# Kernel optimization log

Hardware: AMD Instinct MI355X
Metric: run time of the kernel (lower is better)

The kernel has to match this reference:

```python
import jax, jax.numpy as jnp
import numpy as np

D_DEC = 256  # decoder_size; W columns are [decoder | encoder] per the torch concat order


def setup_inputs() -> dict:
    key = jax.random.key(0)
    k1, k2, k3, k4 = jax.random.split(key, 4)
    B, S, E, D, A = 32, 4096, 256, 256, 256
    decoder_hidden = jax.random.normal(k1, (1, B, D), dtype=jnp.float32)
    encoder_outputs = jax.random.normal(k2, (S, B, E), dtype=jnp.float32)
    W = jax.random.normal(k3, (A, D + E), dtype=jnp.float32) / np.sqrt(D + E)
    b = jax.random.normal(k4, (A,), dtype=jnp.float32) * 0.02
    return {"decoder_hidden": decoder_hidden, "encoder_outputs": encoder_outputs, "W": W, "b": b}


def reference(decoder_hidden, encoder_outputs, W, b):
    # decoder_hidden: [1,B,D] -> [B,D]; encoder_outputs: [S,B,E] -> [B,S,E]
    dh = decoder_hidden[0]
    eo = jnp.transpose(encoder_outputs, (1, 0, 2))
    # Split the concat-linear: cat([dec, enc]) @ W.T == dec @ Wd.T + enc @ We.T
    Wd, We = W[:, :D_DEC], W[:, D_DEC:]
    # scores: tanh(linear) summed over attn dim -> [B,S]
    proj = dh @ Wd.T + b  # [B,A]
    attn = jnp.tanh(proj[:, None, :] + jnp.einsum('bse,ae->bsa', eo, We))
    scores = jnp.sum(attn, axis=2)  # [B,S]
    attn_softmax = jax.nn.softmax(scores, axis=1)  # [B,S]
    attended = jnp.einsum('bs,bse->be', attn_softmax, eo)  # [B,E]
    encoder_norms = jnp.linalg.norm(eo, axis=2)  # [B,S]
    attn_map = attn_softmax * encoder_norms
    return attended, attn_map
```

## Files before the change

### kernel.cpp

```cpp
#include <hip/hip_runtime.h>
#include <math.h>

#define B_  32
#define S_  4096
#define E_  256
#define A_  256
#define DE_ 512

typedef __attribute__((ext_vector_type(8))) short short8;
typedef __attribute__((ext_vector_type(4))) float f32x4;

__device__ inline unsigned short f2bf(float x) {
    unsigned int u = __float_as_uint(x);
    u += 0x7FFFu + ((u >> 16) & 1u);
    return (unsigned short)(u >> 16);
}
__device__ inline float tanh_fast(float x) {
    x = fminf(fmaxf(x, -15.f), 15.f);
    float t = __expf(2.f * x);
    return (t - 1.f) * __builtin_amdgcn_rcpf(t + 1.f);
}

__device__ __forceinline__ void conv_write(float4 v0, float4 v1,
                                           unsigned short* buf, int eu,
                                           unsigned short* rt,
                                           float& nacc)
{
    nacc += v0.x*v0.x + v0.y*v0.y + v0.z*v0.z + v0.w*v0.w
          + v1.x*v1.x + v1.y*v1.y + v1.z*v1.z + v1.w*v1.w;
    float xs[8] = {v0.x, v0.y, v0.z, v0.w, v1.x, v1.y, v1.z, v1.w};
    unsigned int hp[4], lp[4], rp[4];
    #pragma unroll
    for (int j = 0; j < 4; ++j) {
        unsigned int u0 = __float_as_uint(xs[2*j])   & 0xFFFF0000u;
        unsigned int u1 = __float_as_uint(xs[2*j+1]) & 0xFFFF0000u;
        hp[j] = (u0 >> 16) | u1;
        lp[j] = (unsigned int)f2bf(xs[2*j]   - __uint_as_float(u0))
              | ((unsigned int)f2bf(xs[2*j+1] - __uint_as_float(u1)) << 16);
        rp[j] = (unsigned int)f2bf(xs[2*j])
              | ((unsigned int)f2bf(xs[2*j+1]) << 16);
    }
    *(uint4*)&buf[(size_t)eu * 8]         = make_uint4(hp[0], hp[1], hp[2], hp[3]);
    *(uint4*)&buf[(size_t)(264 + eu) * 8] = make_uint4(lp[0], lp[1], lp[2], lp[3]);
    *(uint4*)&rt[(size_t)eu * 8]          = make_uint4(rp[0], rp[1], rp[2], rp[3]);
}

__global__ __launch_bounds__(256) void prep_kernel(
    const float* __restrict__ W, const float* __restrict__ dh,
    const float* __restrict__ bias, unsigned short* __restrict__ wepk,
    float* __restrict__ proj)
{
    __shared__ float dh_lds[E_];
    const int bk  = blockIdx.x;
    const int tid = threadIdx.x;
    if (bk < 64) {
        const int idx = bk * 256 + tid;
        const int c     = idx >> 11;
        const int r     = idx & 2047;
        const int plane = r >> 10;
        const int kg    = (r >> 8) & 3;
        const int a     = r & 255;
        const float* src = W + (size_t)a * DE_ + E_ + c * 32 + kg * 8;
        unsigned int pk[4];
        #pragma unroll
        for (int j = 0; j < 4; ++j) {
            float x0 = src[2 * j], x1 = src[2 * j + 1];
            unsigned int u0 = __float_as_uint(x0) & 0xFFFF0000u;
            unsigned int u1 = __float_as_uint(x1) & 0xFFFF0000u;
            if (plane) {
                unsigned short l0 = f2bf(x0 - __uint_as_float(u0));
                unsigned short l1 = f2bf(x1 - __uint_as_float(u1));
                pk[j] = (unsigned int)l0 | ((unsigned int)l1 << 16);
            } else {
                pk[j] = (u0 >> 16) | u1;
            }
        }
        *(uint4*)&wepk[(size_t)idx * 8] = make_uint4(pk[0], pk[1], pk[2], pk[3]);
    } else {
        const int b = bk - 64;
        const int a = tid;
        dh_lds[a] = dh[b * E_ + a];
        __syncthreads();
        float acc = bias[a];
        const float* wrow = W + (size_t)a * DE_;
        #pragma unroll
        for (int d = 0; d < E_; d += 4) {
            float4 w = *(const float4*)(wrow + d);
            acc += dh_lds[d] * w.x + dh_lds[d+1] * w.y
                 + dh_lds[d+2] * w.z + dh_lds[d+3] * w.w;
        }
        proj[b * A_ + a] = acc;
    }
}

__global__ __launch_bounds__(256, 3) void scores_kernel(
    const float* __restrict__ eo, const unsigned short* __restrict__ wepk,
    const float* __restrict__ proj,
    float* __restrict__ scores, float* __restrict__ nsq,
    float* __restrict__ Pbuf)
{
    __shared__ __align__(16) unsigned char pool[52736];
    unsigned short* eo_hl  = (unsigned short*)pool;
    unsigned short* retain = (unsigned short*)(pool + 18944);

    const int tid = threadIdx.x;
    const int b   = blockIdx.x & (B_ - 1);
    const int s0  = (blockIdx.x >> 5) * 64;
    const int w   = tid >> 6, l = tid & 63;
    const int lq  = l >> 4,  lr = l & 15;

    const int erow = tid >> 2;
    const int ekg  = tid & 3;
    const float* ebase = eo + (size_t)(s0 + erow) * (B_ * E_) + b * E_ + ekg * 8;
    const int eu = ekg * 66 + erow;

    const int wunit = lq * 256 + w * 64 + lr;

    f32x4 acc[4][4];
    #pragma unroll
    for (int i = 0; i < 4; ++i)
        #pragma unroll
        for (int j = 0; j < 4; ++j)
            acc[i][j] = (f32x4){0.f, 0.f, 0.f, 0.f};
    float nacc = 0.f;

    float pr[4];
    #pragma unroll
    for (int nt = 0; nt < 4; ++nt) pr[nt] = proj[b * A_ + w * 64 + nt * 16 + lr];

    {
        float4 v0 = *(const float4*)(ebase);
        float4 v1 = *(const float4*)(ebase + 4);
        conv_write(v0, v1, eo_hl, eu, retain, nacc);
    }
    float4 va0 = *(const float4*)(ebase + 32);
    float4 va1 = *(const float4*)(ebase + 36);
    __syncthreads();

    for (int c = 0; c < 8; ++c) {
        const int p = c & 1;
        unsigned short* rb = eo_hl + (size_t)p * 528 * 8;
        unsigned short* wb = eo_hl + (size_t)(1 - p) * 528 * 8;

        short8 bh[4], bl[4];
        {
            const unsigned short* wsrc = wepk + (size_t)(c * 2048 + wunit) * 8;
            #pragma unroll
            for (int nt = 0; nt < 4; ++nt) {
                bh[nt] = *(const short8*)(wsrc + (size_t)(nt * 16) * 8);
                bl[nt] = *(const short8*)(wsrc + (size_t)(1024 + nt * 16) * 8);
            }
        }
        short8 ah[2], al[2];
        #pragma unroll
        for (int mt = 0; mt < 2; ++mt) {
            const int au = lq * 66 + mt * 16 + lr;
            ah[mt] = *(const short8*)&rb[(size_t)au * 8];
            al[mt] = *(const short8*)&rb[(size_t)(264 + au) * 8];
        }
        if (c < 7) conv_write(va0, va1, wb, eu,
                              retain + (size_t)(c + 1) * 264 * 8, nacc);
        if (c < 6) {
            va0 = *(const float4*)(ebase + (c + 2) * 32);
            va1 = *(const float4*)(ebase + (c + 2) * 32 + 4);
        }
        #pragma unroll
        for (int mt = 0; mt < 2; ++mt) {
            #pragma unroll
            for (int nt = 0; nt < 4; ++nt) {
                acc[mt][nt] = __builtin_amdgcn_mfma_f32_16x16x32_bf16(ah[mt], bh[nt], acc[mt][nt], 0, 0, 0);
                acc[mt][nt] = __builtin_amdgcn_mfma_f32_16x16x32_bf16(ah[mt], bl[nt], acc[mt][nt], 0, 0, 0);
                acc[mt][nt] = __builtin_amdgcn_mfma_f32_16x16x32_bf16(al[mt], bh[nt], acc[mt][nt], 0, 0, 0);
            }
        }
        #pragma unroll
        for (int mt = 2; mt < 4; ++mt) {
            const int au = lq * 66 + mt * 16 + lr;
            short8 ah2 = *(const short8*)&rb[(size_t)au * 8];
            short8 al2 = *(const short8*)&rb[(size_t)(264 + au) * 8];
            #pragma unroll
            for (int nt = 0; nt < 4; ++nt) {
                acc[mt][nt] = __builtin_amdgcn_mfma_f32_16x16x32_bf16(ah2, bh[nt], acc[mt][nt], 0, 0, 0);
                acc[mt][nt] = __builtin_amdgcn_mfma_f32_16x16x32_bf16(ah2, bl[nt], acc[mt][nt], 0, 0, 0);
                acc[mt][nt] = __builtin_amdgcn_mfma_f32_16x16x32_bf16(al2, bh[nt], acc[mt][nt], 0, 0, 0);
            }
        }
        if (c < 7) __syncthreads();
    }
    __syncthreads();

    float* red4  = (float*)pool;
    float* npart = (float*)(pool + 16896);
    float* qpart = (float*)(pool + 17920);
    #pragma unroll
    for (int mt = 0; mt < 4; ++mt) {
        #pragma unroll
        for (int r = 0; r < 4; ++r) {
            float s = 0.f;
            #pragma unroll
            for (int nt = 0; nt < 4; ++nt)
                s += tanh_fast(pr[nt] + acc[mt][nt][r]);
            red4[(w * 16 + lr) * 66 + (mt * 16 + lq * 4 + r)] = s;
        }
    }
    npart[tid] = nacc;
    __syncthreads();
    {
        const int row = tid >> 2, quarter = tid & 3;
        float s = 0.f;
        #pragma unroll
        for (int j = 0; j < 16; ++j) s += red4[(quarter * 16 + j) * 66 + row];
        qpart[quarter * 64 + row] = s;
    }
    __syncthreads();
    float* ws = npart;
    if (tid < 64) {
        const float sc = qpart[tid] + qpart[64 + tid]
                       + qpart[128 + tid] + qpart[192 + tid];
        scores[b * S_ + s0 + tid] = sc;
        nsq[b * S_ + s0 + tid] = npart[4 * tid] + npart[4 * tid + 1]
                               + npart[4 * tid + 2] + npart[4 * tid + 3];
        float mb = sc;
        #pragma unroll
        for (int off = 32; off > 0; off >>= 1)
            mb = fmaxf(mb, __shfl_xor(mb, off, 64));
        const float wv = __expf(sc - mb);
        float zb = wv;
        #pragma unroll
        for (int off = 32; off > 0; off >>= 1)
            zb += __shfl_xor(zb, off, 64);
        ws[tid] = wv;
        if (tid == 0) {
            Pbuf[(size_t)blockIdx.x * 258 + 256] = mb;
            Pbuf[(size_t)blockIdx.x * 258 + 257] = zb;
        }
    }
    __syncthreads();
    {
        const int c2 = tid >> 5, kg2 = (tid >> 3) & 3, j2 = tid & 7;
        const unsigned short* rt = retain + (size_t)(c2 * 264 + kg2 * 66) * 8 + j2;
        float accp = 0.f;
        #pragma unroll 8
        for (int s = 0; s < 64; ++s)
            accp += ws[s] * __uint_as_float((unsigned int)rt[(size_t)s * 8] << 16);
        Pbuf[(size_t)blockIdx.x * 258 + tid] = accp;
    }
}

__global__ __launch_bounds__(256) void stats_kernel(
    const float* __restrict__ scores, const float* __restrict__ nsq,
    float* __restrict__ out)
{
    __shared__ float red[256];
    const int tid  = threadIdx.x;
    const int b    = blockIdx.x & (B_ - 1);
    const int part = blockIdx.x >> 5;
    float v[16];
    float m = -1e30f;
    #pragma unroll
    for (int i = 0; i < 16; ++i) {
        v[i] = scores[b * S_ + i * 256 + tid];
        m = fmaxf(m, v[i]);
    }
    red[tid] = m;
    __syncthreads();
    for (int off = 128; off > 0; off >>= 1) {
        if (tid < off) red[tid] = fmaxf(red[tid], red[tid + off]);
        __syncthreads();
    }
    m = red[0];
    __syncthreads();
    float sum = 0.f;
    #pragma unroll
    for (int i = 0; i < 16; ++i) sum += __expf(v[i] - m);
    red[tid] = sum;
    __syncthreads();
    for (int off = 128; off > 0; off >>= 1) {
        if (tid < off) red[tid] += red[tid + off];
        __syncthreads();
    }
    const float inv = 1.f / red[0];
    #pragma unroll
    for (int j = 0; j < 2; ++j) {
        const int i = part * 2 + j;
        const int s = i * 256 + tid;
        const float pv = __expf(v[i] - m) * inv;
        out[B_ * E_ + b * S_ + s] = pv * sqrtf(nsq[b * S_ + s]);
    }
}

__global__ __launch_bounds__(256) void combine_kernel(
    const float* __restrict__ Pbuf, float* __restrict__ out)
{
    __shared__ float mz[128];
    __shared__ float sc[64];
    const int tid = threadIdx.x;
    const int b   = blockIdx.x;
    if (tid < 64)       mz[tid] = Pbuf[(size_t)(tid * 32 + b) * 258 + 256];
    else if (tid < 128) mz[tid] = Pbuf[(size_t)((tid - 64) * 32 + b) * 258 + 257];
    __syncthreads();
    float m = -1e30f;
    #pragma unroll
    for (int i = 0; i < 64; ++i) m = fmaxf(m, mz[i]);
    float Z = 0.f;
    #pragma unroll
    for (int i = 0; i < 64; ++i) Z += mz[64 + i] * __expf(mz[i] - m);
    if (tid < 64) sc[tid] = __expf(mz[tid] - m);
    __syncthreads();
    float acc = 0.f;
    #pragma unroll 8
    for (int blk = 0; blk < 64; ++blk)
        acc += Pbuf[(size_t)(blk * 32 + b) * 258 + tid] * sc[blk];
    out[b * E_ + tid] = acc / Z;
}

extern "C" void kernel_launch(void* const* d_in, const int* in_sizes, int n_in,
                              void* d_out, int out_size, void* d_ws, size_t ws_size,
                              hipStream_t stream)
{
    const float* dh   = (const float*)d_in[0];
    const float* eo   = (const float*)d_in[1];
    const float* W    = (const float*)d_in[2];
    const float* bias = (const float*)d_in[3];
    float* out = (float*)d_out;
    float* ws  = (float*)d_ws;

    float* projb  = ws;
    float* nsqb   = ws + 8192;
    float* scores = nsqb + S_ * B_;
    float* Pbuf   = scores + S_ * B_;
    unsigned short* wepk = (unsigned short*)(Pbuf + 2048 * 258);

    prep_kernel    <<<96,              256, 0, stream>>>(W, dh, bias, wepk, projb);
    scores_kernel  <<<B_ * (S_ / 64),  256, 0, stream>>>(eo, wepk, projb, scores, nsqb, Pbuf);
    stats_kernel   <<<B_ * 8,          256, 0, stream>>>(scores, nsqb, out);
    combine_kernel <<<B_,              256, 0, stream>>>(Pbuf, out);
}
```

Before: 242.5 us.

## Halve scores tile to 32 rows, load full tile upfront, drop retain buffer

The scores kernel now processes 32 sequence rows per block instead of 64, doubling the grid. It loads and converts the whole 32x256 encoder tile into LDS before the MFMA loop, removing the per-chunk double-buffering and the barriers inside that loop. The separate bf16 retain copy is dropped, and the attended partial sums are rebuilt from the hi+lo split in LDS, which costs less LDS per block and gives better precision. In exchange there is less MFMA work per block, no overlap of global loads with compute, and twice as many partial blocks for the combine kernel to merge.

```diff
diff --git a/kernel.cpp b/kernel.cpp
--- a/kernel.cpp
+++ b/kernel.cpp
@@ -21,15 +21,16 @@
     return (t - 1.f) * __builtin_amdgcn_rcpf(t + 1.f);
 }
 
+#define LO_UNITS 1088
+
 __device__ __forceinline__ void conv_write(float4 v0, float4 v1,
                                            unsigned short* buf, int eu,
-                                           unsigned short* rt,
                                            float& nacc)
 {
     nacc += v0.x*v0.x + v0.y*v0.y + v0.z*v0.z + v0.w*v0.w
           + v1.x*v1.x + v1.y*v1.y + v1.z*v1.z + v1.w*v1.w;
     float xs[8] = {v0.x, v0.y, v0.z, v0.w, v1.x, v1.y, v1.z, v1.w};
-    unsigned int hp[4], lp[4], rp[4];
+    unsigned int hp[4], lp[4];
     #pragma unroll
     for (int j = 0; j < 4; ++j) {
         unsigned int u0 = __float_as_uint(xs[2*j])   & 0xFFFF0000u;
@@ -37,12 +38,9 @@
         hp[j] = (u0 >> 16) | u1;
         lp[j] = (unsigned int)f2bf(xs[2*j]   - __uint_as_float(u0))
               | ((unsigned int)f2bf(xs[2*j+1] - __uint_as_float(u1)) << 16);
-        rp[j] = (unsigned int)f2bf(xs[2*j])
-              | ((unsigned int)f2bf(xs[2*j+1]) << 16);
-    }
-    *(uint4*)&buf[(size_t)eu * 8]         = make_uint4(hp[0], hp[1], hp[2], hp[3]);
-    *(uint4*)&buf[(size_t)(264 + eu) * 8] = make_uint4(lp[0], lp[1], lp[2], lp[3]);
-    *(uint4*)&rt[(size_t)eu * 8]          = make_uint4(rp[0], rp[1], rp[2], rp[3]);
+    }
+    *(uint4*)&buf[(size_t)eu * 8]              = make_uint4(hp[0], hp[1], hp[2], hp[3]);
+    *(uint4*)&buf[(size_t)(LO_UNITS + eu) * 8] = make_uint4(lp[0], lp[1], lp[2], lp[3]);
 }
 
 __global__ __launch_bounds__(256) void prep_kernel(
@@ -99,26 +97,20 @@
     float* __restrict__ scores, float* __restrict__ nsq,
     float* __restrict__ Pbuf)
 {
-    __shared__ __align__(16) unsigned char pool[52736];
-    unsigned short* eo_hl  = (unsigned short*)pool;
-    unsigned short* retain = (unsigned short*)(pool + 18944);
+    __shared__ __align__(16) unsigned char pool[45696];
+    unsigned short* eo_hl = (unsigned short*)pool;
 
     const int tid = threadIdx.x;
     const int b   = blockIdx.x & (B_ - 1);
-    const int s0  = (blockIdx.x >> 5) * 64;
+    const int s0  = (blockIdx.x >> 5) * 32;
     const int w   = tid >> 6, l = tid & 63;
     const int lq  = l >> 4,  lr = l & 15;
 
-    const int erow = tid >> 2;
-    const int ekg  = tid & 3;
-    const float* ebase = eo + (size_t)(s0 + erow) * (B_ * E_) + b * E_ + ekg * 8;
-    const int eu = ekg * 66 + erow;
-
     const int wunit = lq * 256 + w * 64 + lr;
 
-    f32x4 acc[4][4];
-    #pragma unroll
-    for (int i = 0; i < 4; ++i)
+    f32x4 acc[2][4];
+    #pragma unroll
+    for (int i = 0; i < 2; ++i)
         #pragma unroll
         for (int j = 0; j < 4; ++j)
             acc[i][j] = (f32x4){0.f, 0.f, 0.f, 0.f};
@@ -129,107 +121,84 @@
     for (int nt = 0; nt < 4; ++nt) pr[nt] = proj[b * A_ + w * 64 + nt * 16 + lr];
 
     {
-        float4 v0 = *(const float4*)(ebase);
-        float4 v1 = *(const float4*)(ebase + 4);
-        conv_write(v0, v1, eo_hl, eu, retain, nacc);
-    }
-    float4 va0 = *(const float4*)(ebase + 32);
-    float4 va1 = *(const float4*)(ebase + 36);
+        const int sr  = tid >> 3;
+        const int scg = tid & 7;
+        const float* gsrc = eo + (size_t)(s0 + sr) * (B_ * E_) + b * E_ + scg * 32;
+        float4 v[8];
+        #pragma unroll
+        for (int q = 0; q < 8; ++q) v[q] = *(const float4*)(gsrc + q * 4);
+        #pragma unroll
+        for (int kg = 0; kg < 4; ++kg)
+            conv_write(v[2*kg], v[2*kg+1], eo_hl, scg * 136 + kg * 34 + sr, nacc);
+    }
     __syncthreads();
 
     for (int c = 0; c < 8; ++c) {
-        const int p = c & 1;
-        unsigned short* rb = eo_hl + (size_t)p * 528 * 8;
-        unsigned short* wb = eo_hl + (size_t)(1 - p) * 528 * 8;
-
         short8 bh[4], bl[4];
-        {
-            const unsigned short* wsrc = wepk + (size_t)(c * 2048 + wunit) * 8;
+        const unsigned short* wsrc = wepk + ((size_t)c * 2048 + wunit) * 8;
+        #pragma unroll
+        for (int nt = 0; nt < 4; ++nt) {
+            bh[nt] = *(const short8*)(wsrc + (size_t)(nt * 16) * 8);
+            bl[nt] = *(const short8*)(wsrc + (size_t)(1024 + nt * 16) * 8);
+        }
+        #pragma unroll
+        for (int mt = 0; mt < 2; ++mt) {
+            const int au = c * 136 + lq * 34 + mt * 16 + lr;
+            short8 ah = *(const short8*)&eo_hl[(size_t)au * 8];
+            short8 al = *(const short8*)&eo_hl[(size_t)(LO_UNITS + au) * 8];
             #pragma unroll
             for (int nt = 0; nt < 4; ++nt) {
-                bh[nt] = *(const short8*)(wsrc + (size_t)(nt * 16) * 8);
-                bl[nt] = *(const short8*)(wsrc + (size_t)(1024 + nt * 16) * 8);
+                acc[mt][nt] = __builtin_amdgcn_mfma_f32_16x16x32_bf16(ah, bh[nt], acc[mt][nt], 0, 0, 0);
+                acc[mt][nt] = __builtin_amdgcn_mfma_f32_16x16x32_bf16(ah, bl[nt], acc[mt][nt], 0, 0, 0);
+                acc[mt][nt] = __builtin_amdgcn_mfma_f32_16x16x32_bf16(al, bh[nt], acc[mt][nt], 0, 0, 0);
             }
         }
-        short8 ah[2], al[2];
-        #pragma unroll
-        for (int mt = 0; mt < 2; ++mt) {
-            const int au = lq * 66 + mt * 16 + lr;
-            ah[mt] = *(const short8*)&rb[(size_t)au * 8];
-            al[mt] = *(const short8*)&rb[(size_t)(264 + au) * 8];
-        }
-        if (c < 7) conv_write(va0, va1, wb, eu,
-                              retain + (size_t)(c + 1) * 264 * 8, nacc);
-        if (c < 6) {
-            va0 = *(const float4*)(ebase + (c + 2) * 32);
-            va1 = *(const float4*)(ebase + (c + 2) * 32 + 4);
-        }
-        #pragma unroll
-        for (int mt = 0; mt < 2; ++mt) {
-            #pragma unroll
-            for (int nt = 0; nt < 4; ++nt) {
-                acc[mt][nt] = __builtin_amdgcn_mfma_f32_16x16x32_bf16(ah[mt], bh[nt], acc[mt][nt], 0, 0, 0);
-                acc[mt][nt] = __builtin_amdgcn_mfma_f32_16x16x32_bf16(ah[mt], bl[nt], acc[mt][nt], 0, 0, 0);
-                acc[mt][nt] = __builtin_amdgcn_mfma_f32_16x16x32_bf16(al[mt], bh[nt], acc[mt][nt], 0, 0, 0);
-            }
-        }
-        #pragma unroll
-        for (int mt = 2; mt < 4; ++mt) {
-            const int au = lq * 66 + mt * 16 + lr;
-            short8 ah2 = *(const short8*)&rb[(size_t)au * 8];
-            short8 al2 = *(const short8*)&rb[(size_t)(264 + au) * 8];
-            #pragma unroll
-            for (int nt = 0; nt < 4; ++nt) {
-                acc[mt][nt] = __builtin_amdgcn_mfma_f32_16x16x32_bf16(ah2, bh[nt], acc[mt][nt], 0, 0, 0);
-                acc[mt][nt] = __builtin_amdgcn_mfma_f32_16x16x32_bf16(ah2, bl[nt], acc[mt][nt], 0, 0, 0);
-                acc[mt][nt] = __builtin_amdgcn_mfma_f32_16x16x32_bf16(al2, bh[nt], acc[mt][nt], 0, 0, 0);
-            }
-        }
-        if (c < 7) __syncthreads();
-    }
-    __syncthreads();
-
-    float* red4  = (float*)pool;
-    float* npart = (float*)(pool + 16896);
-    float* qpart = (float*)(pool + 17920);
-    #pragma unroll
-    for (int mt = 0; mt < 4; ++mt) {
+    }
+
+    float* red4  = (float*)(pool + 34816);
+    float* npart = (float*)(pool + 43520);
+    float* qpart = (float*)(pool + 44544);
+    float* wsb   = (float*)(pool + 45568);
+    #pragma unroll
+    for (int mt = 0; mt < 2; ++mt) {
         #pragma unroll
         for (int r = 0; r < 4; ++r) {
             float s = 0.f;
             #pragma unroll
             for (int nt = 0; nt < 4; ++nt)
                 s += tanh_fast(pr[nt] + acc[mt][nt][r]);
-            red4[(w * 16 + lr) * 66 + (mt * 16 + lq * 4 + r)] = s;
+            red4[(w * 16 + lr) * 34 + (mt * 16 + lq * 4 + r)] = s;
         }
     }
     npart[tid] = nacc;
     __syncthreads();
     {
-        const int row = tid >> 2, quarter = tid & 3;
+        const int row = tid >> 3, e8 = tid & 7;
         float s = 0.f;
         #pragma unroll
-        for (int j = 0; j < 16; ++j) s += red4[(quarter * 16 + j) * 66 + row];
-        qpart[quarter * 64 + row] = s;
-    }
-    __syncthreads();
-    float* ws = npart;
-    if (tid < 64) {
-        const float sc = qpart[tid] + qpart[64 + tid]
-                       + qpart[128 + tid] + qpart[192 + tid];
+        for (int j = 0; j < 8; ++j) s += red4[(e8 * 8 + j) * 34 + row];
+        qpart[e8 * 32 + row] = s;
+    }
+    __syncthreads();
+    if (tid < 32) {
+        float sc = 0.f;
+        #pragma unroll
+        for (int e = 0; e < 8; ++e) sc += qpart[e * 32 + tid];
         scores[b * S_ + s0 + tid] = sc;
-        nsq[b * S_ + s0 + tid] = npart[4 * tid] + npart[4 * tid + 1]
-                               + npart[4 * tid + 2] + npart[4 * tid + 3];
+        float nn = 0.f;
+        #pragma unroll
+        for (int cc = 0; cc < 8; ++cc) nn += npart[tid * 8 + cc];
+        nsq[b * S_ + s0 + tid] = nn;
         float mb = sc;
         #pragma unroll
-        for (int off = 32; off > 0; off >>= 1)
-            mb = fmaxf(mb, __shfl_xor(mb, off, 64));
+        for (int off = 16; off > 0; off >>= 1)
+            mb = fmaxf(mb, __shfl_xor(mb, off, 32));
         const float wv = __expf(sc - mb);
         float zb = wv;
         #pragma unroll
-        for (int off = 32; off > 0; off >>= 1)
-            zb += __shfl_xor(zb, off, 64);
-        ws[tid] = wv;
+        for (int off = 16; off > 0; off >>= 1)
+            zb += __shfl_xor(zb, off, 32);
+        wsb[tid] = wv;
         if (tid == 0) {
             Pbuf[(size_t)blockIdx.x * 258 + 256] = mb;
             Pbuf[(size_t)blockIdx.x * 258 + 257] = zb;
@@ -237,12 +206,15 @@
     }
     __syncthreads();
     {
-        const int c2 = tid >> 5, kg2 = (tid >> 3) & 3, j2 = tid & 7;
-        const unsigned short* rt = retain + (size_t)(c2 * 264 + kg2 * 66) * 8 + j2;
+        const int pc = tid >> 5, pkg = (tid >> 3) & 3, pj = tid & 7;
+        const int ub = pc * 136 + pkg * 34;
         float accp = 0.f;
         #pragma unroll 8
-        for (int s = 0; s < 64; ++s)
-            accp += ws[s] * __uint_as_float((unsigned int)rt[(size_t)s * 8] << 16);
+        for (int s = 0; s < 32; ++s) {
+            const unsigned int h  = eo_hl[(size_t)(ub + s) * 8 + pj];
+            const unsigned int lo = eo_hl[(size_t)(LO_UNITS + ub + s) * 8 + pj];
+            accp += wsb[s] * (__uint_as_float(h << 16) + __uint_as_float(lo << 16));
+        }
         Pbuf[(size_t)blockIdx.x * 258 + tid] = accp;
     }
 }
@@ -292,24 +264,24 @@
 __global__ __launch_bounds__(256) void combine_kernel(
     const float* __restrict__ Pbuf, float* __restrict__ out)
 {
-    __shared__ float mz[128];
-    __shared__ float sc[64];
+    __shared__ float mz[256];
+    __shared__ float sc[128];
     const int tid = threadIdx.x;
     const int b   = blockIdx.x;
-    if (tid < 64)       mz[tid] = Pbuf[(size_t)(tid * 32 + b) * 258 + 256];
-    else if (tid < 128) mz[tid] = Pbuf[(size_t)((tid - 64) * 32 + b) * 258 + 257];
+    if (tid < 128) mz[tid] = Pbuf[(size_t)(tid * 32 + b) * 258 + 256];
+    else           mz[tid] = Pbuf[(size_t)((tid - 128) * 32 + b) * 258 + 257];
     __syncthreads();
     float m = -1e30f;
     #pragma unroll
-    for (int i = 0; i < 64; ++i) m = fmaxf(m, mz[i]);
+    for (int i = 0; i < 128; ++i) m = fmaxf(m, mz[i]);
     float Z = 0.f;
     #pragma unroll
-    for (int i = 0; i < 64; ++i) Z += mz[64 + i] * __expf(mz[i] - m);
-    if (tid < 64) sc[tid] = __expf(mz[tid] - m);
+    for (int i = 0; i < 128; ++i) Z += mz[128 + i] * __expf(mz[i] - m);
+    if (tid < 128) sc[tid] = __expf(mz[tid] - m);
     __syncthreads();
     float acc = 0.f;
     #pragma unroll 8
-    for (int blk = 0; blk < 64; ++blk)
+    for (int blk = 0; blk < 128; ++blk)
         acc += Pbuf[(size_t)(blk * 32 + b) * 258 + tid] * sc[blk];
     out[b * E_ + tid] = acc / Z;
 }
@@ -329,10 +301,10 @@
     float* nsqb   = ws + 8192;
     float* scores = nsqb + S_ * B_;
     float* Pbuf   = scores + S_ * B_;
-    unsigned short* wepk = (unsigned short*)(Pbuf + 2048 * 258);
-
-    prep_kernel    <<<96,              256, 0, stream>>>(W, dh, bias, wepk, projb);
-    scores_kernel  <<<B_ * (S_ / 64),  256, 0, stream>>>(eo, wepk, projb, scores, nsqb, Pbuf);
-    stats_kernel   <<<B_ * 8,          256, 0, stream>>>(scores, nsqb, out);
-    combine_kernel <<<B_,              256, 0, stream>>>(Pbuf, out);
-}
+    unsigned short* wepk = (unsigned short*)(Pbuf + 4096 * 258);
+
+    prep_kernel    <<<96,             256, 0, stream>>>(W, dh, bias, wepk, projb);
+    scores_kernel  <<<B_ * (S_ / 32), 256, 0, stream>>>(eo, wepk, projb, scores, nsqb, Pbuf);
+    stats_kernel   <<<B_ * 8,         256, 0, stream>>>(scores, nsqb, out);
+    combine_kernel <<<B_,             256, 0, stream>>>(Pbuf, out);
+}
```

New measurement: 281.6 us. +16.1%, slower.

## Double-buffer weight fragments in registers, remap block order, defer proj load

Applied to the files above, without the earlier changes.

The packed We fragments for chunk c+1 are now prefetched into a register double buffer while chunk c's MFMAs run, and the chunk loop is fully unrolled. Previously each chunk's global weight loads sat directly in front of its MFMAs. Block indices are also permuted so consecutive hardware blocks map to different (b, s) tiles, likely to spread work across XCDs or change L2 locality. The proj load moves after the main loop to ease register pressure. The extra register buffers and unrolling risk spilling or lower occupancy under launch_bounds(256,3).

```diff
diff --git a/kernel.cpp b/kernel.cpp
--- a/kernel.cpp
+++ b/kernel.cpp
@@ -104,8 +104,9 @@
     unsigned short* retain = (unsigned short*)(pool + 18944);
 
     const int tid = threadIdx.x;
-    const int b   = blockIdx.x & (B_ - 1);
-    const int s0  = (blockIdx.x >> 5) * 64;
+    const int wg  = ((blockIdx.x & 7) << 8) | (blockIdx.x >> 3);
+    const int b   = wg & (B_ - 1);
+    const int s0  = (wg >> 5) * 64;
     const int w   = tid >> 6, l = tid & 63;
     const int lq  = l >> 4,  lr = l & 15;
 
@@ -124,10 +125,6 @@
             acc[i][j] = (f32x4){0.f, 0.f, 0.f, 0.f};
     float nacc = 0.f;
 
-    float pr[4];
-    #pragma unroll
-    for (int nt = 0; nt < 4; ++nt) pr[nt] = proj[b * A_ + w * 64 + nt * 16 + lr];
-
     {
         float4 v0 = *(const float4*)(ebase);
         float4 v1 = *(const float4*)(ebase + 4);
@@ -135,20 +132,29 @@
     }
     float4 va0 = *(const float4*)(ebase + 32);
     float4 va1 = *(const float4*)(ebase + 36);
-    __syncthreads();
-
+    short8 weh[2][4], wel[2][4];
+    {
+        const unsigned short* ws0 = wepk + (size_t)wunit * 8;
+        #pragma unroll
+        for (int nt = 0; nt < 4; ++nt) {
+            weh[0][nt] = *(const short8*)(ws0 + (size_t)(nt * 16) * 8);
+            wel[0][nt] = *(const short8*)(ws0 + (size_t)(1024 + nt * 16) * 8);
+        }
+    }
+    __syncthreads();
+
+    #pragma unroll
     for (int c = 0; c < 8; ++c) {
-        const int p = c & 1;
-        unsigned short* rb = eo_hl + (size_t)p * 528 * 8;
-        unsigned short* wb = eo_hl + (size_t)(1 - p) * 528 * 8;
-
-        short8 bh[4], bl[4];
-        {
-            const unsigned short* wsrc = wepk + (size_t)(c * 2048 + wunit) * 8;
+        const int cur = c & 1, nxt = cur ^ 1;
+        unsigned short* rb = eo_hl + (size_t)cur * 528 * 8;
+        unsigned short* wb = eo_hl + (size_t)nxt * 528 * 8;
+
+        if (c < 7) {
+            const unsigned short* wsn = wepk + ((size_t)(c + 1) * 2048 + wunit) * 8;
             #pragma unroll
             for (int nt = 0; nt < 4; ++nt) {
-                bh[nt] = *(const short8*)(wsrc + (size_t)(nt * 16) * 8);
-                bl[nt] = *(const short8*)(wsrc + (size_t)(1024 + nt * 16) * 8);
+                weh[nxt][nt] = *(const short8*)(wsn + (size_t)(nt * 16) * 8);
+                wel[nxt][nt] = *(const short8*)(wsn + (size_t)(1024 + nt * 16) * 8);
             }
         }
         short8 ah[2], al[2];
@@ -168,9 +174,9 @@
         for (int mt = 0; mt < 2; ++mt) {
             #pragma unroll
             for (int nt = 0; nt < 4; ++nt) {
-                acc[mt][nt] = __builtin_amdgcn_mfma_f32_16x16x32_bf16(ah[mt], bh[nt], acc[mt][nt], 0, 0, 0);
-                acc[mt][nt] = __builtin_amdgcn_mfma_f32_16x16x32_bf16(ah[mt], bl[nt], acc[mt][nt], 0, 0, 0);
-                acc[mt][nt] = __builtin_amdgcn_mfma_f32_16x16x32_bf16(al[mt], bh[nt], acc[mt][nt], 0, 0, 0);
+                acc[mt][nt] = __builtin_amdgcn_mfma_f32_16x16x32_bf16(ah[mt], weh[cur][nt], acc[mt][nt], 0, 0, 0);
+                acc[mt][nt] = __builtin_amdgcn_mfma_f32_16x16x32_bf16(ah[mt], wel[cur][nt], acc[mt][nt], 0, 0, 0);
+                acc[mt][nt] = __builtin_amdgcn_mfma_f32_16x16x32_bf16(al[mt], weh[cur][nt], acc[mt][nt], 0, 0, 0);
             }
         }
         #pragma unroll
@@ -180,9 +186,9 @@
             short8 al2 = *(const short8*)&rb[(size_t)(264 + au) * 8];
             #pragma unroll
             for (int nt = 0; nt < 4; ++nt) {
-                acc[mt][nt] = __builtin_amdgcn_mfma_f32_16x16x32_bf16(ah2, bh[nt], acc[mt][nt], 0, 0, 0);
-                acc[mt][nt] = __builtin_amdgcn_mfma_f32_16x16x32_bf16(ah2, bl[nt], acc[mt][nt], 0, 0, 0);
-                acc[mt][nt] = __builtin_amdgcn_mfma_f32_16x16x32_bf16(al2, bh[nt], acc[mt][nt], 0, 0, 0);
+                acc[mt][nt] = __builtin_amdgcn_mfma_f32_16x16x32_bf16(ah2, weh[cur][nt], acc[mt][nt], 0, 0, 0);
+                acc[mt][nt] = __builtin_amdgcn_mfma_f32_16x16x32_bf16(ah2, wel[cur][nt], acc[mt][nt], 0, 0, 0);
+                acc[mt][nt] = __builtin_amdgcn_mfma_f32_16x16x32_bf16(al2, weh[cur][nt], acc[mt][nt], 0, 0, 0);
             }
         }
         if (c < 7) __syncthreads();
@@ -192,6 +198,9 @@
     float* red4  = (float*)pool;
     float* npart = (float*)(pool + 16896);
     float* qpart = (float*)(pool + 17920);
+    float pr[4];
+    #pragma unroll
+    for (int nt = 0; nt < 4; ++nt) pr[nt] = proj[b * A_ + w * 64 + nt * 16 + lr];
     #pragma unroll
     for (int mt = 0; mt < 4; ++mt) {
         #pragma unroll
@@ -231,8 +240,8 @@
             zb += __shfl_xor(zb, off, 64);
         ws[tid] = wv;
         if (tid == 0) {
-            Pbuf[(size_t)blockIdx.x * 258 + 256] = mb;
-            Pbuf[(size_t)blockIdx.x * 258 + 257] = zb;
+            Pbuf[(size_t)wg * 258 + 256] = mb;
+            Pbuf[(size_t)wg * 258 + 257] = zb;
         }
     }
     __syncthreads();
@@ -243,7 +252,7 @@
         #pragma unroll 8
         for (int s = 0; s < 64; ++s)
             accp += ws[s] * __uint_as_float((unsigned int)rt[(size_t)s * 8] << 16);
-        Pbuf[(size_t)blockIdx.x * 258 + tid] = accp;
+        Pbuf[(size_t)wg * 258 + tid] = accp;
     }
 }
 
```

Measured after the change: 314.4 us. 1.3x slower.
